# Optimization experiments

Measured on AMD Instinct MI355X. Metric: run time of the kernel, lower is better.

Reference implementation:

```python
import jax, jax.numpy as jnp
import numpy as np


def setup_inputs() -> dict:
    key = jax.random.key(0)
    kp, ka = jax.random.split(key)
    N, A = 100000, 1024
    # points: xyz over a 100m x 100m plot, z in [0, 30] (tree heights)
    u = jax.random.uniform(kp, (N, 3), dtype=jnp.float32)
    points = u * jnp.array([100.0, 100.0, 30.0], dtype=jnp.float32)
    # anchors: [cx, cy, cz, w, l, h]
    ua = jax.random.uniform(ka, (A, 6), dtype=jnp.float32)
    cx = ua[:, 0] * 100.0
    cy = ua[:, 1] * 100.0
    cz = jnp.zeros((A,), jnp.float32)
    w = 2.0 + ua[:, 3] * 6.0
    l = 2.0 + ua[:, 4] * 6.0
    h = 10.0 + ua[:, 5] * 20.0
    anchors = jnp.stack([cx, cy, cz, w, l, h], axis=1)
    return {"points": points, "anchors": anchors, "n": 512}


def _roi_point_pool(points, anchors, n):
    """Vectorised per-anchor point-in-box pooling (TreeRCNN._subsample_points_batch).

    Returns padded [A, n, 3] anchor-local points (x,y translated by anchor
    center, z untouched) and per-anchor clamped counts. Slots >= count are 0.
    Selection of the first-n in-box points is deterministic in point order
    (the torch code uses a random tie-break key; determinism chosen for a
    reproducible correctness baseline — same gather/scatter structure).
    """
    A = anchors.shape[0]
    N = points.shape[0]
    px, py, pz = points[:, 0], points[:, 1], points[:, 2]
    cx, cy = anchors[:, 0:1], anchors[:, 1:2]
    w, l, h = anchors[:, 3:4], anchors[:, 4:5], anchors[:, 5:6]
    # [A, N] box-membership mask (the O(A*N) traffic-bound hot loop)
    mask = ((px >= cx - w * 0.5) & (px <= cx + w * 0.5)
            & (py >= cy - l * 0.5) & (py <= cy + l * 0.5)
            & (pz >= 0.0) & (pz <= h))
    # per-anchor local slot index for each in-box point
    local = jnp.cumsum(mask.astype(jnp.int32), axis=1) - 1          # [A, N]
    valid = mask & (local < n)
    counts = valid.sum(axis=1)                                      # [A]
    # scatter point ids (+1 so 0 marks empty) into flat padded slots;
    # invalid hits go to a dump slot A*n
    flat = jnp.where(valid,
                     jnp.arange(A, dtype=jnp.int32)[:, None] * n + local,
                     A * n)
    vals = (jnp.arange(N, dtype=jnp.int32)[None, :] + 1) * valid
    pid = jnp.zeros(A * n + 1, jnp.int32).at[flat.reshape(-1)].add(vals.reshape(-1))
    pid = pid[: A * n].reshape(A, n)                                # [A, n]
    points_ext = jnp.concatenate([jnp.zeros((1, 3), points.dtype), points], axis=0)
    padded = points_ext[pid]                                        # [A, n, 3]
    # translate x,y to anchor-local coords on filled slots only
    centers = jnp.concatenate([anchors[:, :2], jnp.zeros((A, 1), anchors.dtype)], axis=1)
    padded = jnp.where(pid[..., None] > 0, padded - centers[:, None, :], 0.0)
    return padded, counts


def reference(points, anchors, n):
    return _roi_point_pool(points, anchors, n)
```

## Files before the change

kernel.cpp:

```cpp
#include <hip/hip_runtime.h>


#define NB     128
#define NBB    (NB * NB)
#define CAPB   32
#define NWRD   3584
#define WPT    7
#define MAXBIN 160

__global__ __launch_bounds__(256) void scatter_kernel(
    const float* __restrict__ pts, unsigned int* __restrict__ bincnt,
    float4* __restrict__ bucket, const unsigned int* __restrict__ pbase, int N)
{
    const int i = blockIdx.x * 256 + threadIdx.x;
    if (i >= N) return;
    const unsigned int P = *pbase;
    const float px = pts[3 * i + 0], py = pts[3 * i + 1], pz = pts[3 * i + 2];
    const float s = NB / 100.0f;
    const int bx = min(NB - 1, (int)(px * s));
    const int by = min(NB - 1, (int)(py * s));
    const int bin = by * NB + bx;
    const unsigned int slot = atomicAdd(&bincnt[bin], 1u) - P;
    if (slot < CAPB)
        bucket[bin * CAPB + slot] = make_float4(px, py, pz, __int_as_float(i));
}

__global__ __launch_bounds__(512, 4) void anchor_kernel(
    const float* __restrict__ pts, const float* __restrict__ anc,
    const unsigned int* __restrict__ bincnt, const float4* __restrict__ bucket,
    const unsigned int* __restrict__ pbase,
    float* __restrict__ out_pts, float* __restrict__ out_cnt, int n)
{
    const int a    = blockIdx.x;
    const int tid  = threadIdx.x;
    const int lane = tid & 63;
    const int wave = tid >> 6;

    const float cx = anc[a * 6 + 0], cy = anc[a * 6 + 1];
    const float w  = anc[a * 6 + 3], l  = anc[a * 6 + 4], h = anc[a * 6 + 5];
    const float xl = cx - w * 0.5f, xh = cx + w * 0.5f;
    const float yl = cy - l * 0.5f, yh = cy + l * 0.5f;

    __shared__ unsigned int s_mask[NWRD];
    __shared__ int s_bcnt[MAXBIN];
    __shared__ int s_wsum[8];

    #pragma unroll
    for (int u = 0; u < WPT; ++u) s_mask[tid + u * 512] = 0u;

    const unsigned int P = *pbase;
    const float sc = NB / 100.0f;
    const int bx0 = max(0, (int)floorf(xl * sc));
    const int bx1 = min(NB - 1, (int)floorf(xh * sc));
    const int by0 = max(0, (int)floorf(yl * sc));
    const int by1 = min(NB - 1, (int)floorf(yh * sc));
    const int nbx = bx1 - bx0 + 1;
    const int nby = by1 - by0 + 1;
    const int nbins = (nbx > 0 && nby > 0) ? nbx * nby : 0;

    for (int t = tid; t < nbins; t += 512) {
        const int by = by0 + t / nbx, bx = bx0 + t % nbx;
        s_bcnt[t] = min((int)(bincnt[by * NB + bx] - P), CAPB);
    }

    const int totB = nbins * 8;
    float4 pB0, pB1, pB2, pC0, pC1, pC2;
    {
        const int t0 = tid;
        if (t0 < totB) {
            const int b = t0 >> 3;
            const int off = ((by0 + b / nbx) * NB + bx0 + b % nbx) * CAPB + (t0 & 7);
            pB0 = bucket[off];
            pC0 = bucket[off + 8];
        }
        const int t1 = tid + 512;
        if (t1 < totB) {
            const int b = t1 >> 3;
            const int off = ((by0 + b / nbx) * NB + bx0 + b % nbx) * CAPB + (t1 & 7);
            pB1 = bucket[off];
            pC1 = bucket[off + 8];
        }
        const int t2 = tid + 1024;
        if (t2 < totB) {
            const int b = t2 >> 3;
            const int off = ((by0 + b / nbx) * NB + bx0 + b % nbx) * CAPB + (t2 & 7);
            pB2 = bucket[off];
            pC2 = bucket[off + 8];
        }
    }
    __syncthreads();

    {
        const int t0 = tid;
        if (t0 < totB) {
            const int cnt = s_bcnt[t0 >> 3];
            const int sl  = t0 & 7;
            if (sl < cnt &&
                pB0.x >= xl && pB0.x <= xh && pB0.y >= yl && pB0.y <= yh &&
                pB0.z >= 0.0f && pB0.z <= h) {
                const int idx = __float_as_int(pB0.w);
                atomicOr(&s_mask[idx >> 5], 1u << (idx & 31));
            }
            if (sl + 8 < cnt &&
                pC0.x >= xl && pC0.x <= xh && pC0.y >= yl && pC0.y <= yh &&
                pC0.z >= 0.0f && pC0.z <= h) {
                const int idx = __float_as_int(pC0.w);
                atomicOr(&s_mask[idx >> 5], 1u << (idx & 31));
            }
        }
        const int t1 = tid + 512;
        if (t1 < totB) {
            const int cnt = s_bcnt[t1 >> 3];
            const int sl  = t1 & 7;
            if (sl < cnt &&
                pB1.x >= xl && pB1.x <= xh && pB1.y >= yl && pB1.y <= yh &&
                pB1.z >= 0.0f && pB1.z <= h) {
                const int idx = __float_as_int(pB1.w);
                atomicOr(&s_mask[idx >> 5], 1u << (idx & 31));
            }
            if (sl + 8 < cnt &&
                pC1.x >= xl && pC1.x <= xh && pC1.y >= yl && pC1.y <= yh &&
                pC1.z >= 0.0f && pC1.z <= h) {
                const int idx = __float_as_int(pC1.w);
                atomicOr(&s_mask[idx >> 5], 1u << (idx & 31));
            }
        }
        const int t2 = tid + 1024;
        if (t2 < totB) {
            const int cnt = s_bcnt[t2 >> 3];
            const int sl  = t2 & 7;
            if (sl < cnt &&
                pB2.x >= xl && pB2.x <= xh && pB2.y >= yl && pB2.y <= yh &&
                pB2.z >= 0.0f && pB2.z <= h) {
                const int idx = __float_as_int(pB2.w);
                atomicOr(&s_mask[idx >> 5], 1u << (idx & 31));
            }
            if (sl + 8 < cnt &&
                pC2.x >= xl && pC2.x <= xh && pC2.y >= yl && pC2.y <= yh &&
                pC2.z >= 0.0f && pC2.z <= h) {
                const int idx = __float_as_int(pC2.w);
                atomicOr(&s_mask[idx >> 5], 1u << (idx & 31));
            }
        }
    }

    const int totC = nbins * 16;
    for (int t = tid; t < totC; t += 512) {
        const int b    = t >> 4;
        const int slot = 16 + (t & 15);
        const int cnt  = s_bcnt[b];
        if (slot < cnt) {
            const int bin  = (by0 + b / nbx) * NB + bx0 + b % nbx;
            const float4 p = bucket[bin * CAPB + slot];
            if (p.x >= xl && p.x <= xh && p.y >= yl && p.y <= yh &&
                p.z >= 0.0f && p.z <= h) {
                const int idx = __float_as_int(p.w);
                atomicOr(&s_mask[idx >> 5], 1u << (idx & 31));
            }
        }
    }
    __syncthreads();

    const int wbase = tid * WPT;
    int s = 0;
    unsigned int mw[WPT];
    #pragma unroll
    for (int u = 0; u < WPT; ++u) {
        mw[u] = s_mask[wbase + u];
        s += __popc(mw[u]);
    }
    int incl = s;
    #pragma unroll
    for (int d = 1; d < 64; d <<= 1) {
        const int t = __shfl_up(incl, d);
        if (lane >= d) incl += t;
    }
    if (lane == 63) s_wsum[wave] = incl;
    __syncthreads();

    int pre = 0, total = 0;
    #pragma unroll
    for (int v = 0; v < 8; ++v) {
        const int t = s_wsum[v];
        if (v < wave) pre += t;
        total += t;
    }
    const int count = total < n ? total : n;
    int slot = pre + incl - s;

    float* const outa = out_pts + (size_t)a * n * 3;
    #pragma unroll
    for (int u = 0; u < WPT; ++u) {
        unsigned int wm = mw[u];
        while (wm) {
            const int b = __ffs(wm) - 1;
            wm &= wm - 1u;
            if (slot < n) {
                const int i = (wbase + u) * 32 + b;
                outa[3 * slot + 0] = pts[3 * i + 0] - cx;
                outa[3 * slot + 1] = pts[3 * i + 1] - cy;
                outa[3 * slot + 2] = pts[3 * i + 2];
            }
            ++slot;
        }
    }

    for (int t = count * 3 + tid; t < n * 3; t += 512) outa[t] = 0.f;
    if (tid == 0) out_cnt[a] = (float)count;
}

__global__ __launch_bounds__(256) void roi_pool_kernel(
    const float* __restrict__ pts, const float* __restrict__ anc,
    float* __restrict__ out_pts, float* __restrict__ out_cnt, int N, int n)
{
    const int a = blockIdx.x;
    const float cx = anc[a * 6 + 0], cy = anc[a * 6 + 1];
    const float w  = anc[a * 6 + 3], l  = anc[a * 6 + 4], h = anc[a * 6 + 5];
    const float xmin = cx - 0.5f * w, xmax = cx + 0.5f * w;
    const float ymin = cy - 0.5f * l, ymax = cy + 0.5f * l;
    const int tid = threadIdx.x, wave = tid >> 6, lane = tid & 63;
    __shared__ int s_tot[4];
    int base = 0;
    float* const outa = out_pts + (size_t)a * n * 3;
    for (int start = 0; start < N; start += 256) {
        const int i = start + tid;
        bool m = false;
        float px = 0.f, py = 0.f, pz = 0.f;
        if (i < N) {
            px = pts[3 * i]; py = pts[3 * i + 1]; pz = pts[3 * i + 2];
            m = (px >= xmin) & (px <= xmax) & (py >= ymin) & (py <= ymax) &
                (pz >= 0.0f) & (pz <= h);
        }
        const unsigned long long ball = __ballot(m);
        const int lanePfx = __popcll(ball & ((1ull << lane) - 1ull));
        if (lane == 0) s_tot[wave] = __popcll(ball);
        __syncthreads();
        const int t0 = s_tot[0], t1 = s_tot[1], t2 = s_tot[2], t3 = s_tot[3];
        int offs = base;
        if (wave > 0) offs += t0;
        if (wave > 1) offs += t1;
        if (wave > 2) offs += t2;
        const int slot = offs + lanePfx;
        if (m && slot < n) {
            float* o = outa + (size_t)slot * 3;
            o[0] = px - cx; o[1] = py - cy; o[2] = pz;
        }
        base += t0 + t1 + t2 + t3;
        __syncthreads();
        if (base >= n) break;
    }
    const int count = base < n ? base : n;
    if (tid == 0) out_cnt[a] = (float)count;
    for (int s = count + tid; s < n; s += 256) {
        float* o = outa + (size_t)s * 3;
        o[0] = 0.f; o[1] = 0.f; o[2] = 0.f;
    }
}

extern "C" void kernel_launch(void* const* d_in, const int* in_sizes, int n_in,
                              void* d_out, int out_size, void* d_ws, size_t ws_size,
                              hipStream_t stream) {
    const float* pts = (const float*)d_in[0];
    const float* anc = (const float*)d_in[1];
    const int N = in_sizes[0] / 3;
    const int A = in_sizes[1] / 6;
    const int n = (out_size / A - 1) / 3;

    float* out_pts = (float*)d_out;
    float* out_cnt = (float*)d_out + (size_t)A * n * 3;

    const size_t bucket_bytes = (size_t)NBB * CAPB * sizeof(float4);
    const size_t cnt_bytes    = (size_t)NBB * sizeof(int);
    const size_t total_ws     = bucket_bytes + cnt_bytes + 64;

    if (ws_size < total_ws || N > NWRD * 32) {
        roi_pool_kernel<<<dim3(A), dim3(256), 0, stream>>>(pts, anc, out_pts, out_cnt, N, n);
        return;
    }

    float4* bucket       = (float4*)d_ws;
    unsigned int* bincnt = (unsigned int*)((char*)d_ws + bucket_bytes);
    const unsigned int* pbase =
        (const unsigned int*)((char*)d_ws + bucket_bytes + cnt_bytes);

    const int pb = (N + 255) / 256;

    scatter_kernel<<<dim3(pb), dim3(256), 0, stream>>>(pts, bincnt, bucket, pbase, N);
    anchor_kernel<<<dim3(A), dim3(512), 0, stream>>>(pts, anc, bincnt, bucket, pbase,
                                                     out_pts, out_cnt, n);
}
```

Before: 75.41 us.

## Emit pooled points in parallel by rank from register-held bucket candidates

Builds a per-word exclusive prefix array in shared memory, then has every thread that holds an in-box candidate compute its output rank from the word prefix plus a masked popcount and write it directly. This replaces the serial per-thread bit-scan loop over mask words that re-read point coordinates from global memory. Candidates from the overflow slots (16 and up) are reloaded from the bucket. The cost is a second shared array of mask size, one extra barrier, and the box test done twice.

After: 72.23 us, median of 2. 1.04x faster.

```diff
diff --git a/kernel.cpp b/kernel.cpp
--- a/kernel.cpp
+++ b/kernel.cpp
@@ -26,7 +26,7 @@
 }
 
 __global__ __launch_bounds__(512, 4) void anchor_kernel(
-    const float* __restrict__ pts, const float* __restrict__ anc,
+    const float* __restrict__ anc,
     const unsigned int* __restrict__ bincnt, const float4* __restrict__ bucket,
     const unsigned int* __restrict__ pbase,
     float* __restrict__ out_pts, float* __restrict__ out_cnt, int n)
@@ -42,6 +42,7 @@
     const float yl = cy - l * 0.5f, yh = cy + l * 0.5f;
 
     __shared__ unsigned int s_mask[NWRD];
+    __shared__ unsigned int s_wpre[NWRD];
     __shared__ int s_bcnt[MAXBIN];
     __shared__ int s_wsum[8];
 
@@ -90,20 +91,18 @@
     }
     __syncthreads();
 
+    #define TESTP(p) ((p).x >= xl && (p).x <= xh && (p).y >= yl && \
+                      (p).y <= yh && (p).z >= 0.0f && (p).z <= h)
     {
         const int t0 = tid;
         if (t0 < totB) {
             const int cnt = s_bcnt[t0 >> 3];
             const int sl  = t0 & 7;
-            if (sl < cnt &&
-                pB0.x >= xl && pB0.x <= xh && pB0.y >= yl && pB0.y <= yh &&
-                pB0.z >= 0.0f && pB0.z <= h) {
+            if (sl < cnt && TESTP(pB0)) {
                 const int idx = __float_as_int(pB0.w);
                 atomicOr(&s_mask[idx >> 5], 1u << (idx & 31));
             }
-            if (sl + 8 < cnt &&
-                pC0.x >= xl && pC0.x <= xh && pC0.y >= yl && pC0.y <= yh &&
-                pC0.z >= 0.0f && pC0.z <= h) {
+            if (sl + 8 < cnt && TESTP(pC0)) {
                 const int idx = __float_as_int(pC0.w);
                 atomicOr(&s_mask[idx >> 5], 1u << (idx & 31));
             }
@@ -112,15 +111,11 @@
         if (t1 < totB) {
             const int cnt = s_bcnt[t1 >> 3];
             const int sl  = t1 & 7;
-            if (sl < cnt &&
-                pB1.x >= xl && pB1.x <= xh && pB1.y >= yl && pB1.y <= yh &&
-                pB1.z >= 0.0f && pB1.z <= h) {
+            if (sl < cnt && TESTP(pB1)) {
                 const int idx = __float_as_int(pB1.w);
                 atomicOr(&s_mask[idx >> 5], 1u << (idx & 31));
             }
-            if (sl + 8 < cnt &&
-                pC1.x >= xl && pC1.x <= xh && pC1.y >= yl && pC1.y <= yh &&
-                pC1.z >= 0.0f && pC1.z <= h) {
+            if (sl + 8 < cnt && TESTP(pC1)) {
                 const int idx = __float_as_int(pC1.w);
                 atomicOr(&s_mask[idx >> 5], 1u << (idx & 31));
             }
@@ -129,15 +124,11 @@
         if (t2 < totB) {
             const int cnt = s_bcnt[t2 >> 3];
             const int sl  = t2 & 7;
-            if (sl < cnt &&
-                pB2.x >= xl && pB2.x <= xh && pB2.y >= yl && pB2.y <= yh &&
-                pB2.z >= 0.0f && pB2.z <= h) {
+            if (sl < cnt && TESTP(pB2)) {
                 const int idx = __float_as_int(pB2.w);
                 atomicOr(&s_mask[idx >> 5], 1u << (idx & 31));
             }
-            if (sl + 8 < cnt &&
-                pC2.x >= xl && pC2.x <= xh && pC2.y >= yl && pC2.y <= yh &&
-                pC2.z >= 0.0f && pC2.z <= h) {
+            if (sl + 8 < cnt && TESTP(pC2)) {
                 const int idx = __float_as_int(pC2.w);
                 atomicOr(&s_mask[idx >> 5], 1u << (idx & 31));
             }
@@ -148,12 +139,10 @@
     for (int t = tid; t < totC; t += 512) {
         const int b    = t >> 4;
         const int slot = 16 + (t & 15);
-        const int cnt  = s_bcnt[b];
-        if (slot < cnt) {
+        if (slot < s_bcnt[b]) {
             const int bin  = (by0 + b / nbx) * NB + bx0 + b % nbx;
             const float4 p = bucket[bin * CAPB + slot];
-            if (p.x >= xl && p.x <= xh && p.y >= yl && p.y <= yh &&
-                p.z >= 0.0f && p.z <= h) {
+            if (TESTP(p)) {
                 const int idx = __float_as_int(p.w);
                 atomicOr(&s_mask[idx >> 5], 1u << (idx & 31));
             }
@@ -186,24 +175,61 @@
         total += t;
     }
     const int count = total < n ? total : n;
-    int slot = pre + incl - s;
+
+    unsigned int run = (unsigned int)(pre + incl - s);
+    #pragma unroll
+    for (int u = 0; u < WPT; ++u) {
+        s_wpre[wbase + u] = run;
+        run += (unsigned int)__popc(mw[u]);
+    }
+    __syncthreads();
 
     float* const outa = out_pts + (size_t)a * n * 3;
-    #pragma unroll
-    for (int u = 0; u < WPT; ++u) {
-        unsigned int wm = mw[u];
-        while (wm) {
-            const int b = __ffs(wm) - 1;
-            wm &= wm - 1u;
-            if (slot < n) {
-                const int i = (wbase + u) * 32 + b;
-                outa[3 * slot + 0] = pts[3 * i + 0] - cx;
-                outa[3 * slot + 1] = pts[3 * i + 1] - cy;
-                outa[3 * slot + 2] = pts[3 * i + 2];
-            }
-            ++slot;
-        }
-    }
+    #define EMITP(p) do {                                                    \
+        const int idx = __float_as_int((p).w);                               \
+        const int wd  = idx >> 5;                                            \
+        const int rank = (int)s_wpre[wd] +                                   \
+            __popc(s_mask[wd] & ((1u << (idx & 31)) - 1u));                  \
+        if (rank < n) {                                                      \
+            outa[3 * rank + 0] = (p).x - cx;                                 \
+            outa[3 * rank + 1] = (p).y - cy;                                 \
+            outa[3 * rank + 2] = (p).z;                                      \
+        }                                                                    \
+    } while (0)
+    {
+        const int t0 = tid;
+        if (t0 < totB) {
+            const int cnt = s_bcnt[t0 >> 3];
+            const int sl  = t0 & 7;
+            if (sl < cnt && TESTP(pB0)) EMITP(pB0);
+            if (sl + 8 < cnt && TESTP(pC0)) EMITP(pC0);
+        }
+        const int t1 = tid + 512;
+        if (t1 < totB) {
+            const int cnt = s_bcnt[t1 >> 3];
+            const int sl  = t1 & 7;
+            if (sl < cnt && TESTP(pB1)) EMITP(pB1);
+            if (sl + 8 < cnt && TESTP(pC1)) EMITP(pC1);
+        }
+        const int t2 = tid + 1024;
+        if (t2 < totB) {
+            const int cnt = s_bcnt[t2 >> 3];
+            const int sl  = t2 & 7;
+            if (sl < cnt && TESTP(pB2)) EMITP(pB2);
+            if (sl + 8 < cnt && TESTP(pC2)) EMITP(pC2);
+        }
+    }
+    for (int t = tid; t < totC; t += 512) {
+        const int b    = t >> 4;
+        const int slot = 16 + (t & 15);
+        if (slot < s_bcnt[b]) {
+            const int bin  = (by0 + b / nbx) * NB + bx0 + b % nbx;
+            const float4 p = bucket[bin * CAPB + slot];
+            if (TESTP(p)) EMITP(p);
+        }
+    }
+    #undef TESTP
+    #undef EMITP
 
     for (int t = count * 3 + tid; t < n * 3; t += 512) outa[t] = 0.f;
     if (tid == 0) out_cnt[a] = (float)count;
@@ -286,6 +312,6 @@
     const int pb = (N + 255) / 256;
 
     scatter_kernel<<<dim3(pb), dim3(256), 0, stream>>>(pts, bincnt, bucket, pbase, N);
-    anchor_kernel<<<dim3(A), dim3(512), 0, stream>>>(pts, anc, bincnt, bucket, pbase,
+    anchor_kernel<<<dim3(A), dim3(512), 0, stream>>>(anc, bincnt, bucket, pbase,
                                                      out_pts, out_cnt, n);
 }
```
